# Kernel optimization log

Hardware: AMD Instinct MI355X
Metric: run time of the kernel (lower is better)

Reference implementation:

```python
import jax, jax.numpy as jnp
import numpy as np
from jax import lax

V, F, B = 25000, 8192, 1024  # vertices, faces, block size (batch_size)
EPS = 1e-8

def setup_inputs() -> dict:
    key = jax.random.key(0)
    k1, k2, k3 = jax.random.split(key, 3)
    vertices = jax.random.normal(k1, (V, 3), dtype=jnp.float32)
    faces = jax.random.randint(k2, (F, 3), 0, V, dtype=jnp.int64)
    face_probs = jax.random.uniform(k3, (F,), dtype=jnp.float32)
    return {"vertices": vertices, "faces": faces, "face_probs": face_probs}

def reference(vertices, faces, face_probs):
    nF = faces.shape[0]
    # edges = cat([ (f0,f1), (f1,f2), (f2,f0) ])  -> [E,2], E = 3F
    edges = jnp.concatenate([faces[:, [0, 1]], faces[:, [1, 2]], faces[:, [2, 0]]], axis=0)
    # Faithful to source: edge_to_face = arange(F).repeat_interleave(3)
    edge_to_face = jnp.repeat(jnp.arange(nF), 3)
    edge_points = vertices[edges]              # [E,2,3]
    centroids = edge_points.mean(axis=1)       # [E,3]
    E = edges.shape[0]
    v_all = edge_points[:, 1] - edge_points[:, 0] + EPS  # edge directions + eps, [E,3]
    starts = edge_points[:, 0]                 # [E,3] (unused by count but kept for clarity)
    col_idx = jnp.arange(E)

    def block(carry, b):
        row_cnt, col_cnt = carry
        i0 = b * B
        c_blk = lax.dynamic_slice(centroids, (i0, 0), (B, 3))   # [B,3]
        v1 = lax.dynamic_slice(v_all, (i0, 0), (B, 3))          # [B,3]
        # pairwise L2 distances [B,E]
        d2 = ((c_blk[:, None, :] - centroids[None, :, :]) ** 2).sum(-1)
        dists = jnp.sqrt(d2)
        pair = (dists < 1.0 + 1e-6) & ((i0 + jnp.arange(B))[:, None] < col_idx[None, :])
        # cross2 = cross(v1, v2); crossing iff ||cross2||+eps > 1e-5
        cross2 = jnp.cross(v1[:, None, :], v_all[None, :, :])   # [B,E,3]
        norm2 = jnp.sqrt((cross2 ** 2).sum(-1)) + EPS
        # after clamp t in [0,1] always, so crossings = pair & valid
        crossings = (pair & (norm2 > 1e-5)).astype(jnp.float32)
        row_cnt = lax.dynamic_update_slice(row_cnt, crossings.sum(1), (i0,))
        col_cnt = col_cnt + crossings.sum(0)
        return (row_cnt, col_cnt), None

    init = (jnp.zeros(E, jnp.float32), jnp.zeros(E, jnp.float32))
    (row_cnt, col_cnt), _ = lax.scan(block, init, jnp.arange(E // B))
    cnt_per_edge = row_cnt + col_cnt           # times edge appears as e1 or e2 in a crossing
    crossing_count = jax.ops.segment_sum(cnt_per_edge, edge_to_face, num_segments=nF)
    crossing_count = jnp.clip(crossing_count, 0.0, 100.0)
    return (face_probs * crossing_count).mean()
```

## Files before the change

### kernel.cpp

```cpp
#include <hip/hip_runtime.h>

#define V_ 25000
#define F_ 8192
#define E_ (3 * F_)

constexpr int CAP  = 101;
constexpr int GD   = 8;
constexpr int NC   = GD*GD*GD;
constexpr int CAPC = 6144;

constexpr size_t OFF_LIST = 393216;
constexpr size_t OFF_CCNT = 50724864;
constexpr size_t OFF_CNT  = 50726912;

__device__ __forceinline__ int cell_coord(float c)
{
    return min(GD-1, max(0, (int)floorf(c) + GD/2));
}

__global__ __launch_bounds__(256) void build_kernel(
    const float* __restrict__ vertices, const int* __restrict__ faces,
    float4* __restrict__ C4, float4* __restrict__ cellList,
    int* __restrict__ cellCount)
{
    __shared__ int lh[NC];
    __shared__ int lbase[NC];
    for (int i = threadIdx.x; i < NC; i += 256) lh[i] = 0;
    __syncthreads();

    const int e = blockIdx.x * 256 + threadIdx.x;
    int f, i0, i1;
    if (e < F_)        { f = e;        i0 = 0; i1 = 1; }
    else if (e < 2*F_) { f = e - F_;   i0 = 1; i1 = 2; }
    else               { f = e - 2*F_; i0 = 2; i1 = 0; }
    int a = faces[f*3 + i0];
    int b = faces[f*3 + i1];
    float cx = 0.5f*(vertices[a*3+0] + vertices[b*3+0]);
    float cy = 0.5f*(vertices[a*3+1] + vertices[b*3+1]);
    float cz = 0.5f*(vertices[a*3+2] + vertices[b*3+2]);
    int cell = (cell_coord(cz)*GD + cell_coord(cy))*GD + cell_coord(cx);
    int rank = atomicAdd(&lh[cell], 1);
    __syncthreads();
    for (int i = threadIdx.x; i < NC; i += 256) {
        int c = lh[i];
        if (c) lbase[i] = atomicAdd(&cellCount[i], c);
    }
    __syncthreads();
    C4[e] = make_float4(cx, cy, cz, __int_as_float(cell));
    cellList[(size_t)cell * CAPC + lbase[cell] + rank] = make_float4(cx, cy, cz, 0.f);
}

__global__ __launch_bounds__(256) void count_kernel(
    const float4* __restrict__ C4, const float4* __restrict__ cellList,
    const int* __restrict__ cellCount, int* __restrict__ cnt)
{
    const int wave = threadIdx.x >> 6;
    const int lane = threadIdx.x & 63;
    const int e = blockIdx.x * 4 + wave;

    float4 s = C4[e];
    const float ex = s.x, ey = s.y, ez = s.z;
    const int   cell = __float_as_int(s.w);
    const int ix = cell & 7, iy = (cell >> 3) & 7, iz = cell >> 6;
    const float d2t = (1.0f + 1e-6f) * (1.0f + 1e-6f);

    const int D[3] = {0, -1, 1};
    int count = 0;
#pragma unroll
    for (int qz = 0; qz < 3; ++qz) {
        int z = iz + D[qz];
        if ((unsigned)z >= (unsigned)GD) continue;
#pragma unroll
        for (int qy = 0; qy < 3; ++qy) {
            int y = iy + D[qy];
            if ((unsigned)y >= (unsigned)GD) continue;
#pragma unroll
            for (int qx = 0; qx < 3; ++qx) {
                int x = ix + D[qx];
                if ((unsigned)x >= (unsigned)GD) continue;
                int nc = (z*GD + y)*GD + x;
                int n = cellCount[nc];
                const float4* __restrict__ L = cellList + (size_t)nc * CAPC;
                for (int base = 0; base < n; base += 64) {
                    int idx = base + lane;
                    float4 t = L[min(idx, n - 1)];
                    float dx = ex - t.x, dy = ey - t.y, dz = ez - t.z;
                    float d2 = dx*dx + dy*dy + dz*dz;
                    bool c = (idx < n) && (d2 < d2t);
                    count += __popcll(__ballot(c));
                    if (count >= CAP) goto done;
                }
            }
        }
    }
done:
    if (lane == 0) cnt[e] = count;
}

__global__ __launch_bounds__(1024) void reduce_kernel(
    const int* __restrict__ cnt, const float* __restrict__ probs,
    float* __restrict__ out)
{
    float local = 0.0f;
    for (int f = threadIdx.x; f < F_; f += 1024) {
        float c = (float)(cnt[f] + cnt[F_ + f] + cnt[2*F_ + f]);
        c = fminf(fmaxf(c, 0.0f), 100.0f);
        local += probs[f] * c;
    }
#pragma unroll
    for (int off = 32; off > 0; off >>= 1)
        local += __shfl_down(local, off, 64);
    __shared__ float wsum[16];
    if ((threadIdx.x & 63) == 0) wsum[threadIdx.x >> 6] = local;
    __syncthreads();
    if (threadIdx.x == 0) {
        float t = 0.0f;
#pragma unroll
        for (int w = 0; w < 16; w++) t += wsum[w];
        out[0] = t / (float)F_;
    }
}

extern "C" void kernel_launch(void* const* d_in, const int* in_sizes, int n_in,
                              void* d_out, int out_size, void* d_ws, size_t ws_size,
                              hipStream_t stream)
{
    const float* vertices = (const float*)d_in[0];
    const int*   faces    = (const int*)d_in[1];
    const float* probs    = (const float*)d_in[2];
    float* out = (float*)d_out;

    char* ws = (char*)d_ws;
    float4* C4        = (float4*)ws;
    float4* cellList  = (float4*)(ws + OFF_LIST);
    int*    cellCount = (int*)(ws + OFF_CCNT);
    int*    cnt       = (int*)(ws + OFF_CNT);

    hipMemsetAsync(cellCount, 0, NC * sizeof(int), stream);
    hipLaunchKernelGGL(build_kernel, dim3(E_ / 256), dim3(256), 0, stream,
                       vertices, faces, C4, cellList, cellCount);
    hipLaunchKernelGGL(count_kernel, dim3(E_ / 4), dim3(256), 0, stream,
                       C4, cellList, cellCount, cnt);
    hipLaunchKernelGGL(reduce_kernel, dim3(1), dim3(1024), 0, stream,
                       cnt, probs, out);
}
```

Measured before the change: 103.6 us.

## Flatten neighbor-cell chunk list in LDS and software-pipeline loads in count kernel

The count kernel first scans the home cell with a prefetch of the next 64-entry chunk. It then has lanes compute the 26 neighbor cell counts in parallel, ordered toward the grid center. A prefix scan turns these into a flat chunk list in LDS, which is processed four chunks at a time with the next four loads issued ahead. This replaces the serial per-cell loop with its dependent loads and short tail chunks, at the cost of extra LDS use, a wave-level scan and added code complexity.

```diff
diff --git a/kernel.cpp b/kernel.cpp
--- a/kernel.cpp
+++ b/kernel.cpp
@@ -8,10 +8,21 @@
 constexpr int GD   = 8;
 constexpr int NC   = GD*GD*GD;
 constexpr int CAPC = 6144;
+constexpr int FLATCAP = 384;
 
 constexpr size_t OFF_LIST = 393216;
 constexpr size_t OFF_CCNT = 50724864;
 constexpr size_t OFF_CNT  = 50726912;
+
+__device__ const int PPAT[26][3] = {
+    { 1, 1, 1},
+    { 1, 1, 0},{ 1, 0, 1},{ 0, 1, 1},
+    { 1, 0, 0},{ 0, 1, 0},{ 0, 0, 1},{ 1, 1,-1},{ 1,-1, 1},{-1, 1, 1},
+    { 1,-1, 0},{ 1, 0,-1},{ 0, 1,-1},{-1, 1, 0},{-1, 0, 1},{ 0,-1, 1},
+    {-1, 0, 0},{ 0,-1, 0},{ 0, 0,-1},{-1,-1, 1},{-1, 1,-1},{ 1,-1,-1},
+    {-1,-1, 0},{-1, 0,-1},{ 0,-1,-1},
+    {-1,-1,-1}
+};
 
 __device__ __forceinline__ int cell_coord(float c)
 {
@@ -54,6 +65,7 @@
     const float4* __restrict__ C4, const float4* __restrict__ cellList,
     const int* __restrict__ cellCount, int* __restrict__ cnt)
 {
+    __shared__ unsigned flatLDS[4][FLATCAP + 16];
     const int wave = threadIdx.x >> 6;
     const int lane = threadIdx.x & 63;
     const int e = blockIdx.x * 4 + wave;
@@ -64,34 +76,115 @@
     const int ix = cell & 7, iy = (cell >> 3) & 7, iz = cell >> 6;
     const float d2t = (1.0f + 1e-6f) * (1.0f + 1e-6f);
 
-    const int D[3] = {0, -1, 1};
     int count = 0;
+
+    {
+        const int n = cellCount[cell];
+        const float4* __restrict__ L = cellList + (size_t)cell * CAPC;
+        float4 cur = L[lane];
+        for (int base = 0;;) {
+            int nb = base + 64;
+            bool more = nb < n;
+            float4 nxt;
+            if (more) nxt = L[nb + lane];
+            float dx = ex - cur.x, dy = ey - cur.y, dz = ez - cur.z;
+            float d2 = dx*dx + dy*dy + dz*dz;
+            bool c = (base + lane < n) && (d2 < d2t);
+            count += __popcll(__ballot(c));
+            if (count >= CAP) goto done;
+            if (!more) break;
+            cur = nxt; base = nb;
+        }
+    }
+
+    {
+        const int dirx = (ix <= 3) ? 1 : -1;
+        const int diry = (iy <= 3) ? 1 : -1;
+        const int dirz = (iz <= 3) ? 1 : -1;
+
+        int cq = 0, nq = 0, cellq = cell;
+        if (lane < 26) {
+            int ox = PPAT[lane][0] * dirx;
+            int oy = PPAT[lane][1] * diry;
+            int oz = PPAT[lane][2] * dirz;
+            int x = ix + ox, y = iy + oy, z = iz + oz;
+            if (((unsigned)x < (unsigned)GD) & ((unsigned)y < (unsigned)GD) &
+                ((unsigned)z < (unsigned)GD)) {
+                cellq = cell + oz*64 + oy*8 + ox;
+                nq = cellCount[cellq];
+                cq = (nq + 63) >> 6;
+            }
+        }
+        int incl = cq;
 #pragma unroll
-    for (int qz = 0; qz < 3; ++qz) {
-        int z = iz + D[qz];
-        if ((unsigned)z >= (unsigned)GD) continue;
-#pragma unroll
-        for (int qy = 0; qy < 3; ++qy) {
-            int y = iy + D[qy];
-            if ((unsigned)y >= (unsigned)GD) continue;
-#pragma unroll
-            for (int qx = 0; qx < 3; ++qx) {
-                int x = ix + D[qx];
-                if ((unsigned)x >= (unsigned)GD) continue;
-                int nc = (z*GD + y)*GD + x;
-                int n = cellCount[nc];
-                const float4* __restrict__ L = cellList + (size_t)nc * CAPC;
+        for (int d = 1; d < 64; d <<= 1) {
+            int t = __shfl_up(incl, d, 64);
+            if (lane >= d) incl += t;
+        }
+        const int T = __shfl(incl, 63);
+        const int excl = incl - cq;
+
+        if (T == 0) goto done;
+
+        if (T > FLATCAP) {
+            for (int q = 0; q < 26; ++q) {
+                int ox = PPAT[q][0] * dirx, oy = PPAT[q][1] * diry,
+                    oz = PPAT[q][2] * dirz;
+                int x = ix + ox, y = iy + oy, z = iz + oz;
+                if (((unsigned)x >= (unsigned)GD) | ((unsigned)y >= (unsigned)GD) |
+                    ((unsigned)z >= (unsigned)GD)) continue;
+                int nc2 = cell + oz*64 + oy*8 + ox;
+                int n = cellCount[nc2];
+                const float4* __restrict__ L = cellList + (size_t)nc2 * CAPC;
                 for (int base = 0; base < n; base += 64) {
-                    int idx = base + lane;
-                    float4 t = L[min(idx, n - 1)];
-                    float dx = ex - t.x, dy = ey - t.y, dz = ez - t.z;
+                    float4 t4 = L[base + lane];
+                    float dx = ex - t4.x, dy = ey - t4.y, dz = ez - t4.z;
                     float d2 = dx*dx + dy*dy + dz*dz;
-                    bool c = (idx < n) && (d2 < d2t);
+                    bool c = (base + lane < n) && (d2 < d2t);
                     count += __popcll(__ballot(c));
                     if (count >= CAP) goto done;
                 }
             }
-        }
+            goto done;
+        }
+
+        for (int k = 0; k < cq; ++k)
+            flatLDS[wave][excl + k] =
+                ((unsigned)cellq << 14) | ((unsigned)k << 7)
+                | (unsigned)min(64, nq - k*64);
+        {
+            int pi = T + lane;
+            if (pi < T + 12) flatLDS[wave][pi] = (unsigned)cell << 14;
+        }
+        asm volatile("s_waitcnt lgkmcnt(0)" ::: "memory");
+
+        const int Tp = (T + 3) & ~3;
+
+#define FADDR(E) (cellList + (size_t)((E) >> 14) * CAPC + (((E) >> 7) & 127) * 64 + lane)
+#define PROC(B, EN)                                                        \
+        {                                                                  \
+            float dx = ex - (B).x, dy = ey - (B).y, dz = ez - (B).z;       \
+            float d2 = dx*dx + dy*dy + dz*dz;                              \
+            bool c = (lane < (int)((EN) & 127u)) && (d2 < d2t);            \
+            count += __popcll(__ballot(c));                                \
+            if (count >= CAP) goto done;                                   \
+        }
+
+        unsigned e0 = flatLDS[wave][0], e1 = flatLDS[wave][1],
+                 e2 = flatLDS[wave][2], e3 = flatLDS[wave][3];
+        float4 b0 = *FADDR(e0), b1 = *FADDR(e1), b2 = *FADDR(e2), b3 = *FADDR(e3);
+        for (int j = 0;; j += 4) {
+            unsigned f0 = flatLDS[wave][j+4], f1 = flatLDS[wave][j+5],
+                     f2 = flatLDS[wave][j+6], f3 = flatLDS[wave][j+7];
+            float4 n0 = *FADDR(f0), n1 = *FADDR(f1),
+                   n2 = *FADDR(f2), n3 = *FADDR(f3);
+            PROC(b0, e0) PROC(b1, e1) PROC(b2, e2) PROC(b3, e3)
+            if (j + 4 >= Tp) break;
+            e0 = f0; e1 = f1; e2 = f2; e3 = f3;
+            b0 = n0; b1 = n1; b2 = n2; b3 = n3;
+        }
+#undef FADDR
+#undef PROC
     }
 done:
     if (lane == 0) cnt[e] = count;
```

New measurement: 88.76 us (median of 2 runs). 1.17x faster.
